# Optimization experiments

Measured on AMD Instinct MI355X. Metric: run time of the kernel, lower is better.

## Reference

```python
import jax, jax.numpy as jnp
import numpy as np

NUM_HEADS = 8
EPS = 1e-5


def setup_inputs() -> dict:
    key = jax.random.key(0)
    ks = jax.random.split(key, 7)
    B, C, H, W, D = 1, 256, 16, 16, 16
    return {
        "x": jax.random.normal(ks[0], (B, C, H, W, D), dtype=jnp.float32),
        "w_dw": jax.random.normal(ks[1], (C, 1, 3, 3, 3), dtype=jnp.float32) * 0.05,
        "b_dw": jax.random.normal(ks[2], (C,), dtype=jnp.float32) * 0.05,
        "w_qkv": jax.random.normal(ks[3], (3 * C, C), dtype=jnp.float32) * 0.05,
        "b_qkv": jax.random.normal(ks[4], (3 * C,), dtype=jnp.float32) * 0.05,
        "w_proj": jax.random.normal(ks[5], (C, C), dtype=jnp.float32) * 0.05,
        "b_proj": jax.random.normal(ks[6], (C,), dtype=jnp.float32) * 0.05,
    }


def reference(x, w_dw, b_dw, w_qkv, b_qkv, w_proj, b_proj):
    B, C, H, W, D = x.shape
    nh = NUM_HEADS
    hd = C // nh
    scale = hd ** (-0.5)
    N = H * W * D

    # depthwise 3x3x3 conv (groups=C), SAME padding
    y = jax.lax.conv_general_dilated(
        x, w_dw, window_strides=(1, 1, 1), padding="SAME",
        dimension_numbers=("NCHWD", "OIHWD", "NCHWD"),
        feature_group_count=C,
    ) + b_dw[None, :, None, None, None]

    # InstanceNorm3d (affine=False): normalize over spatial dims per (b, c)
    mu = y.mean(axis=(2, 3, 4), keepdims=True)
    var = y.var(axis=(2, 3, 4), keepdims=True)
    y = (y - mu) * jax.lax.rsqrt(var + EPS)

    # 1x1x1 conv -> 3*C channels
    qkv = jnp.einsum("bchwd,oc->bohwd", y, w_qkv) + b_qkv[None, :, None, None, None]

    # [B, 3, nh, hd, N] -> q, k, v each [B, nh, N, hd]
    qkv = qkv.reshape(B, 3, nh, hd, N)
    q, k, v = jnp.transpose(qkv, (1, 0, 2, 4, 3))

    attn = jax.nn.softmax(jnp.einsum("bhnd,bhmd->bhnm", q, k) * scale, axis=-1)
    out = jnp.einsum("bhnm,bhmd->bhnd", attn, v)  # [B, nh, N, hd]

    # transpose(-1, -2) then reshape to [B, C, H, W, D]
    out = jnp.transpose(out, (0, 1, 3, 2)).reshape(B, C, H, W, D)

    # output 1x1x1 projection
    out = jnp.einsum("bchwd,oc->bohwd", out, w_proj) + b_proj[None, :, None, None, None]
    return out
```

## Files before the change

kernel.cpp:

```cpp
#include <hip/hip_runtime.h>
#include <hip/hip_bf16.h>

#define NSP 4096
#define QSC2 0.25503486f

typedef __attribute__((ext_vector_type(8))) short bf16x8;
typedef __attribute__((ext_vector_type(4))) float f32x4;
typedef __attribute__((ext_vector_type(16))) float f32x16;

__device__ __forceinline__ unsigned short f2bf(float f){
  union{float f;unsigned int u;}c; c.f=f;
  unsigned int r = c.u + 0x7fffu + ((c.u>>16)&1u);
  return (unsigned short)(r>>16);
}
__device__ __forceinline__ unsigned int pk2(float a, float b){
  __hip_bfloat162 p = __float22bfloat162_rn(make_float2(a, b));
  unsigned int r; __builtin_memcpy(&r, &p, 4); return r;
}
__device__ __forceinline__ ushort4 pk4(float a, float b, float c, float d){
  union { ushort4 u4; uint2 u2; } u;
  u.u2.x = pk2(a, b); u.u2.y = pk2(c, d);
  return u.u4;
}
__device__ __forceinline__ float bfu2f(unsigned short u){
  union { unsigned int i; float f; } c; c.i = ((unsigned int)u) << 16; return c.f;
}

__global__ __launch_bounds__(1024) void k_dwconv(
    const float* __restrict__ x,
    const float* __restrict__ wdw,
    unsigned short* __restrict__ ybn)
{
  const int c = blockIdx.x;
  const int tid = threadIdx.x;
  __shared__ float xs[4096];
  __shared__ float wsh[27];
  __shared__ float rs[16], rq[16];

  const float* xc = x + (size_t)c * NSP;
  *(float4*)&xs[tid*4] = ((const float4*)xc)[tid];
  if (tid < 27) wsh[tid] = wdw[c*27 + tid];
  __syncthreads();

  const int h = tid >> 6, w = (tid >> 2) & 15, d0 = (tid & 3) * 4;
  float acc[4] = {};
  #pragma unroll
  for (int kh = 0; kh < 3; kh++){
    const int hh = h + kh - 1;
    if ((unsigned)hh >= 16u) continue;
    #pragma unroll
    for (int kw = 0; kw < 3; kw++){
      const int ww = w + kw - 1;
      if ((unsigned)ww >= 16u) continue;
      const float* rowp = &xs[((hh << 4) + ww) << 4];
      float win[6];
      const float4 c0 = *(const float4*)&rowp[d0];
      win[1] = c0.x; win[2] = c0.y; win[3] = c0.z; win[4] = c0.w;
      win[0] = d0        ? rowp[d0 - 1] : 0.f;
      win[5] = (d0 < 12) ? rowp[d0 + 4] : 0.f;
      #pragma unroll
      for (int kd = 0; kd < 3; kd++){
        const float wv = wsh[kh*9 + kw*3 + kd];
        #pragma unroll
        for (int j = 0; j < 4; j++) acc[j] += wv * win[j + kd];
      }
    }
  }

  float sum = 0.f, sumsq = 0.f;
  #pragma unroll
  for (int j = 0; j < 4; j++){ sum += acc[j]; sumsq += acc[j]*acc[j]; }
  #pragma unroll
  for (int off = 32; off > 0; off >>= 1){
    sum   += __shfl_down(sum, off, 64);
    sumsq += __shfl_down(sumsq, off, 64);
  }
  const int wid = tid >> 6, lane = tid & 63;
  if (lane == 0){ rs[wid] = sum; rq[wid] = sumsq; }
  __syncthreads();
  float ts = 0.f, tq = 0.f;
  #pragma unroll
  for (int i = 0; i < 16; i++){ ts += rs[i]; tq += rq[i]; }
  const float mean = ts * (1.f/4096.f);
  const float var  = tq * (1.f/4096.f) - mean*mean;
  const float rinv = rsqrtf(var + 1e-5f);

  *(ushort4*)(ybn + (size_t)c * NSP + tid*4) =
      pk4((acc[0]-mean)*rinv, (acc[1]-mean)*rinv, (acc[2]-mean)*rinv, (acc[3]-mean)*rinv);
}

__global__ __launch_bounds__(256) void k_qkv(
    const float* __restrict__ wqkv,
    const float* __restrict__ bqkv,
    const unsigned short* __restrict__ ybn,
    unsigned short* __restrict__ qb, unsigned short* __restrict__ kb,
    unsigned short* __restrict__ vbt)
{
  __shared__ unsigned short Wb[64][264];
  __shared__ unsigned short Ys[64][264];
  __shared__ float bsh[64];
  const int tid = threadIdx.x;
  const int o0 = blockIdx.y * 64;
  const int n0 = blockIdx.x * 64;
  {
    const int row = tid & 63, part = tid >> 6;
    const float* src = wqkv + (size_t)(o0 + row) * 256 + part * 64;
    unsigned short* dst = &Wb[row][part*64];
    #pragma unroll
    for (int j = 0; j < 8; j++){
      const float4 a = ((const float4*)src)[2*j];
      const float4 b = ((const float4*)src)[2*j+1];
      *(ushort4*)&dst[j*8]     = pk4(a.x, a.y, a.z, a.w);
      *(ushort4*)&dst[j*8 + 4] = pk4(b.x, b.y, b.z, b.w);
    }
    if (tid < 64) bsh[tid] = bqkv[o0 + tid];
  }
  {
    const int cl = tid >> 4, n4 = (tid & 15) * 4;
    #pragma unroll
    for (int i = 0; i < 16; i++){
      const int c = cl * 16 + i;
      const ushort4 v = *(const ushort4*)(ybn + (size_t)c * NSP + n0 + n4);
      Ys[n4+0][c] = v.x; Ys[n4+1][c] = v.y; Ys[n4+2][c] = v.z; Ys[n4+3][c] = v.w;
    }
  }
  __syncthreads();

  const int w = tid >> 6, lane = tid & 63, quad = lane >> 4, cc = lane & 15;
  const int nbase = n0 + w*16;
  const bool isv = (o0 >= 512);
  f32x4 acc[4] = {};

  #pragma unroll
  for (int k = 0; k < 8; k++){
    const bf16x8 y0 = *(const bf16x8*)&Ys[w*16 + cc][k*32 + quad*8];
    #pragma unroll
    for (int os = 0; os < 4; os++){
      const bf16x8 wf = *(const bf16x8*)&Wb[os*16 + cc][k*32 + quad*8];
      if (!isv) acc[os] = __builtin_amdgcn_mfma_f32_16x16x32_bf16(wf, y0, acc[os], 0, 0, 0);
      else      acc[os] = __builtin_amdgcn_mfma_f32_16x16x32_bf16(y0, wf, acc[os], 0, 0, 0);
    }
  }

  if (!isv){
    #pragma unroll
    for (int os = 0; os < 4; os++){
      const int obase = o0 + os*16 + quad*4;
      const int g = obase >> 8, hh = (obase >> 5) & 7, dd0 = obase & 31;
      const int n = nbase + cc;
      unsigned short* dst = (g == 0) ? qb : kb;
      const float sc = (g == 0) ? QSC2 : 1.f;
      const int bb = os*16 + quad*4;
      *(ushort4*)&dst[((size_t)hh * NSP + n) * 32 + dd0] =
          pk4((acc[os][0] + bsh[bb+0]) * sc, (acc[os][1] + bsh[bb+1]) * sc,
              (acc[os][2] + bsh[bb+2]) * sc, (acc[os][3] + bsh[bb+3]) * sc);
    }
  } else {
    #pragma unroll
    for (int os = 0; os < 4; os++){
      const int orow = o0 - 512 + os*16 + cc;
      const float bias = bsh[os*16 + cc];
      const int n4 = nbase + quad*4;
      *(ushort4*)&vbt[(size_t)orow * NSP + n4] =
          pk4(acc[os][0] + bias, acc[os][1] + bias, acc[os][2] + bias, acc[os][3] + bias);
    }
  }
}

__global__ __launch_bounds__(256) void k_attn(
    const unsigned short* __restrict__ qb,
    const unsigned short* __restrict__ kb,
    const unsigned short* __restrict__ vbt,
    unsigned short* __restrict__ opb, float* __restrict__ lp, int ktlen)
{
  const int h = blockIdx.y, q0 = blockIdx.x * 128, z = blockIdx.z;
  const int tid = threadIdx.x;
  const int w = tid >> 6, l = tid & 63;
  const int lq = l & 31, lb = l >> 5;

  __shared__ unsigned short ks [64][40];
  __shared__ unsigned short vsT[32][72];
  __shared__ unsigned short pst[128][72];

  const int qg = q0 + w*32 + lq;
  const bf16x8 qf0 = *(const bf16x8*)(qb + ((size_t)(h*NSP + qg))*32 + lb*8);
  const bf16x8 qf1 = *(const bf16x8*)(qb + ((size_t)(h*NSP + qg))*32 + 16 + lb*8);
  const unsigned short* kbase = kb  + (size_t)h * NSP * 32;
  const unsigned short* vbase = vbt + (size_t)h * 32 * NSP;

  f32x16 oacc = {};
  float lsum = 0.f;

  const int kt0 = z * ktlen;
  const int krow = tid >> 2, kseg = (tid & 3) * 8;
  const int vrow = tid >> 3, vseg = (tid & 7) * 8;
  const int iters = ktlen >> 6;

  for (int it = 0; it < iters; it++){
    const int kt = kt0 + it * 64;
    {
      *(uint4*)&ks[krow][kseg]  = *(const uint4*)(kbase + (size_t)(kt + krow) * 32 + kseg);
      *(uint4*)&vsT[vrow][vseg] = *(const uint4*)(vbase + (size_t)vrow * NSP + kt + vseg);
    }
    __syncthreads();

    #pragma unroll
    for (int t2 = 0; t2 < 2; t2++){
      const bf16x8 af0 = *(const bf16x8*)&ks[t2*32 + lq][lb*8];
      const bf16x8 af1 = *(const bf16x8*)&ks[t2*32 + lq][16 + lb*8];
      f32x16 sa = {};
      sa = __builtin_amdgcn_mfma_f32_32x32x16_bf16(af0, qf0, sa, 0, 0, 0);
      sa = __builtin_amdgcn_mfma_f32_32x32x16_bf16(af1, qf1, sa, 0, 0, 0);
      #pragma unroll
      for (int g = 0; g < 4; g++){
        const float p0 = __builtin_amdgcn_exp2f(sa[g*4+0]);
        const float p1 = __builtin_amdgcn_exp2f(sa[g*4+1]);
        const float p2 = __builtin_amdgcn_exp2f(sa[g*4+2]);
        const float p3 = __builtin_amdgcn_exp2f(sa[g*4+3]);
        lsum += (p0 + p1) + (p2 + p3);
        *(ushort4*)&pst[w*32 + lq][t2*32 + g*8 + lb*4] = pk4(p0, p1, p2, p3);
      }
    }
    #pragma unroll
    for (int ck = 0; ck < 4; ck++){
      const bf16x8 vf = *(const bf16x8*)&vsT[lq]       [ck*16 + lb*8];
      const bf16x8 pf = *(const bf16x8*)&pst[w*32 + lq][ck*16 + lb*8];
      oacc = __builtin_amdgcn_mfma_f32_32x32x16_bf16(vf, pf, oacc, 0, 0, 0);
    }
    __syncthreads();
  }

  lsum += __shfl_xor(lsum, 32, 64);

  unsigned short* dst = opb + ((size_t)z * NSP + qg) * 256 + h*32;
  #pragma unroll
  for (int g = 0; g < 4; g++){
    *(ushort4*)(dst + g*8 + lb*4) =
        pk4(oacc[g*4+0], oacc[g*4+1], oacc[g*4+2], oacc[g*4+3]);
  }
  if (lb == 0) lp[((size_t)z * 8 + h) * NSP + qg] = lsum;
}

__global__ __launch_bounds__(256) void k_proj(
    const float* __restrict__ wproj,
    const float* __restrict__ bproj,
    const unsigned short* __restrict__ opb,
    const float* __restrict__ lp,
    float* __restrict__ out, int nz)
{
  __shared__ unsigned short Wb[32][264];
  const int tid = threadIdx.x;
  const int o0 = blockIdx.y * 32;
  const int n0 = blockIdx.x * 64;
  {
    const int row = tid & 31, part = tid >> 5;
    const float* src = wproj + (size_t)(o0 + row) * 256 + part * 32;
    unsigned short* dst = &Wb[row][part*32];
    #pragma unroll
    for (int j = 0; j < 4; j++){
      const float4 a = ((const float4*)src)[2*j];
      const float4 b = ((const float4*)src)[2*j+1];
      *(ushort4*)&dst[j*8]     = pk4(a.x, a.y, a.z, a.w);
      *(ushort4*)&dst[j*8 + 4] = pk4(b.x, b.y, b.z, b.w);
    }
  }
  __syncthreads();

  const int w = tid >> 6, lane = tid & 63, quad = lane >> 4, cc = lane & 15;
  const int nbase = n0 + w*16;
  const int nr = nbase + cc;
  f32x4 acc[2] = {};

  #pragma unroll
  for (int k = 0; k < 8; k++){
    float lt = 0.f;
    float s[8] = {};
    for (int z = 0; z < nz; z++){
      lt += lp[((size_t)z*8 + k) * NSP + nr];
      union { uint4 q; unsigned short u[8]; } v;
      v.q = *(const uint4*)(opb + ((size_t)z * NSP + nr) * 256 + k*32 + quad*8);
      #pragma unroll
      for (int j = 0; j < 8; j++) s[j] += bfu2f(v.u[j]);
    }
    const float r = 1.f / lt;
    union { bf16x8 v; ushort4 u[2]; } yb;
    yb.u[0] = pk4(s[0]*r, s[1]*r, s[2]*r, s[3]*r);
    yb.u[1] = pk4(s[4]*r, s[5]*r, s[6]*r, s[7]*r);
    #pragma unroll
    for (int os = 0; os < 2; os++){
      const bf16x8 wf = *(const bf16x8*)&Wb[os*16 + cc][k*32 + quad*8];
      acc[os] = __builtin_amdgcn_mfma_f32_16x16x32_bf16(yb.v, wf, acc[os], 0, 0, 0);
    }
  }

  #pragma unroll
  for (int os = 0; os < 2; os++){
    const int o = o0 + os*16 + cc;
    const float bias = bproj[o];
    const int n4 = nbase + quad*4;
    *(float4*)&out[(size_t)o * NSP + n4] =
        make_float4(acc[os][0] + bias, acc[os][1] + bias,
                    acc[os][2] + bias, acc[os][3] + bias);
  }
}

extern "C" void kernel_launch(void* const* d_in, const int* in_sizes, int n_in,
                              void* d_out, int out_size, void* d_ws, size_t ws_size,
                              hipStream_t stream) {
  (void)in_sizes; (void)n_in; (void)out_size;
  const float* x     = (const float*)d_in[0];
  const float* wdw   = (const float*)d_in[1];
  const float* bdw   = (const float*)d_in[2];  (void)bdw;
  const float* wqkv  = (const float*)d_in[3];
  const float* bqkv  = (const float*)d_in[4];
  const float* wproj = (const float*)d_in[5];
  const float* bproj = (const float*)d_in[6];
  float* out = (float*)d_out;

  const int nz = (ws_size >= ((size_t)16 << 20)) ? 4 : 2;
  const int ktlen = NSP / nz;

  char* ws = (char*)d_ws;
  const size_t opB = (size_t)nz << 21;
  unsigned short* opb = (unsigned short*)ws;
  unsigned short* ybn = (unsigned short*)ws;
  unsigned short* qb  = (unsigned short*)(ws + opB);
  unsigned short* kb  = (unsigned short*)(ws + opB + (2<<20));
  unsigned short* vbt = (unsigned short*)(ws + opB + (4<<20));
  float*          lp  = (float*)(ws + opB + (6<<20));

  k_dwconv <<<dim3(256),        dim3(1024), 0, stream>>>(x, wdw, ybn);
  k_qkv    <<<dim3(64, 12),     dim3(256),  0, stream>>>(wqkv, bqkv, ybn, qb, kb, vbt);
  k_attn   <<<dim3(32, 8, nz),  dim3(256),  0, stream>>>(qb, kb, vbt, opb, lp, ktlen);
  k_proj   <<<dim3(64, 8),      dim3(256),  0, stream>>>(wproj, bproj, opb, lp, out, nz);
}
```

Before: 140.5 us.

## Fuse all stages into one cooperative persistent kernel with grid syncs

Replaces the four separate launches with a single cooperative kernel of 512 blocks that runs depthwise conv, instance-norm stats, QKV GEMM, attention and projection as phases separated by grid-wide syncs. The conv is split across two blocks per channel, with partial stats exchanged through global memory. The aim is to remove per-launch overhead and inter-kernel gaps. In exchange it adds grid barrier costs and caps parallelism at 512 resident blocks, so attention tasks are looped per block. It falls back to the old four launches if the cooperative launch fails.

```diff
diff --git a/kernel.cpp b/kernel.cpp
--- a/kernel.cpp
+++ b/kernel.cpp
@@ -1,5 +1,8 @@
 #include <hip/hip_runtime.h>
 #include <hip/hip_bf16.h>
+#include <hip/hip_cooperative_groups.h>
+
+namespace cg = cooperative_groups;
 
 #define NSP 4096
 #define QSC2 0.25503486f
@@ -26,9 +29,291 @@
   union { unsigned int i; float f; } c; c.i = ((unsigned int)u) << 16; return c.f;
 }
 
+struct FParams {
+  const float* x; const float* wdw;
+  const float* wqkv; const float* bqkv;
+  const float* wproj; const float* bproj;
+  unsigned short* ybn; unsigned short* qb; unsigned short* kb; unsigned short* vbt;
+  unsigned short* opb; float* lp; float2* stats;
+  float* out; int nz; int ktlen;
+};
+
+__global__ __launch_bounds__(256) void k_fused(FParams p)
+{
+  __shared__ __align__(16) char smem[67840];
+  cg::grid_group gg = cg::this_grid();
+  const int tid = threadIdx.x;
+  const int bid = blockIdx.x;
+  const int w = tid >> 6, lane = tid & 63, quad = lane >> 4, cc = lane & 15;
+
+  float a8[8];
+  {
+    float* xs  = (float*)smem;
+    float* wsh = (float*)(smem + 16384);
+    float* rs  = (float*)(smem + 16512);
+    float* rq  = (float*)(smem + 16544);
+    const int c = bid >> 1, half = bid & 1;
+    const float* xc = p.x + (size_t)c * NSP;
+    #pragma unroll
+    for (int i = 0; i < 4; i++)
+      *(float4*)&xs[(i*256 + tid)*4] = ((const float4*)xc)[i*256 + tid];
+    if (tid < 27) wsh[tid] = p.wdw[c*27 + tid];
+    __syncthreads();
+
+    const int h = half*8 + (tid >> 5), ww0 = (tid >> 1) & 15, d0 = (tid & 1) * 8;
+    #pragma unroll
+    for (int j = 0; j < 8; j++) a8[j] = 0.f;
+    #pragma unroll
+    for (int kh = 0; kh < 3; kh++){
+      const int hh = h + kh - 1;
+      if ((unsigned)hh >= 16u) continue;
+      #pragma unroll
+      for (int kw = 0; kw < 3; kw++){
+        const int ww = ww0 + kw - 1;
+        if ((unsigned)ww >= 16u) continue;
+        const float* rowp = &xs[((hh << 4) + ww) << 4];
+        float win[10];
+        const float4 c0 = *(const float4*)&rowp[d0];
+        const float4 c1 = *(const float4*)&rowp[d0 + 4];
+        win[1] = c0.x; win[2] = c0.y; win[3] = c0.z; win[4] = c0.w;
+        win[5] = c1.x; win[6] = c1.y; win[7] = c1.z; win[8] = c1.w;
+        win[0] = d0 ? rowp[7] : 0.f;
+        win[9] = d0 ? 0.f : rowp[8];
+        #pragma unroll
+        for (int kd = 0; kd < 3; kd++){
+          const float wv = wsh[kh*9 + kw*3 + kd];
+          #pragma unroll
+          for (int j = 0; j < 8; j++) a8[j] += wv * win[j + kd];
+        }
+      }
+    }
+    float sum = 0.f, sumsq = 0.f;
+    #pragma unroll
+    for (int j = 0; j < 8; j++){ sum += a8[j]; sumsq += a8[j]*a8[j]; }
+    #pragma unroll
+    for (int off = 32; off > 0; off >>= 1){
+      sum   += __shfl_down(sum, off, 64);
+      sumsq += __shfl_down(sumsq, off, 64);
+    }
+    if (lane == 0){ rs[w] = sum; rq[w] = sumsq; }
+    __syncthreads();
+    if (tid == 0)
+      p.stats[bid] = make_float2(rs[0]+rs[1]+rs[2]+rs[3], rq[0]+rq[1]+rq[2]+rq[3]);
+  }
+  gg.sync();
+
+  {
+    const int c = bid >> 1, half = bid & 1;
+    const float2 s0 = p.stats[bid & ~1], s1 = p.stats[bid | 1];
+    const float mean = (s0.x + s1.x) * (1.f/4096.f);
+    const float var  = (s0.y + s1.y) * (1.f/4096.f) - mean*mean;
+    const float rinv = rsqrtf(var + 1e-5f);
+    const int h = half*8 + (tid >> 5), ww0 = (tid >> 1) & 15, d0 = (tid & 1) * 8;
+    unsigned short* yo = p.ybn + (size_t)c * NSP + (h << 8) + (ww0 << 4) + d0;
+    *(ushort4*)yo =
+        pk4((a8[0]-mean)*rinv, (a8[1]-mean)*rinv, (a8[2]-mean)*rinv, (a8[3]-mean)*rinv);
+    *(ushort4*)(yo + 4) =
+        pk4((a8[4]-mean)*rinv, (a8[5]-mean)*rinv, (a8[6]-mean)*rinv, (a8[7]-mean)*rinv);
+  }
+  gg.sync();
+
+  {
+    unsigned short (*Ys)[264] = (unsigned short (*)[264])smem;
+    unsigned short (*Wb)[264] = (unsigned short (*)[264])(smem + 33792);
+    float* bsh = (float*)(smem + 67584);
+    const int nt = bid >> 3, oslot = bid & 7;
+    const int n0 = nt * 64;
+    {
+      const int cl = tid >> 4, n4 = (tid & 15) * 4;
+      #pragma unroll
+      for (int i = 0; i < 16; i++){
+        const int c = cl*16 + i;
+        const ushort4 v = *(const ushort4*)(p.ybn + (size_t)c * NSP + n0 + n4);
+        Ys[n4+0][c] = v.x; Ys[n4+1][c] = v.y; Ys[n4+2][c] = v.z; Ys[n4+3][c] = v.w;
+      }
+    }
+    const int numo = (oslot < 4) ? 2 : 1;
+    for (int oi = 0; oi < numo; oi++){
+      const int o0 = (oslot + oi*8) * 64;
+      __syncthreads();
+      {
+        const int row = tid & 63, part = tid >> 6;
+        const float* src = p.wqkv + (size_t)(o0 + row) * 256 + part * 64;
+        unsigned short* dst = &Wb[row][part*64];
+        #pragma unroll
+        for (int j = 0; j < 8; j++){
+          const float4 a = ((const float4*)src)[2*j];
+          const float4 b = ((const float4*)src)[2*j+1];
+          *(ushort4*)&dst[j*8]     = pk4(a.x, a.y, a.z, a.w);
+          *(ushort4*)&dst[j*8 + 4] = pk4(b.x, b.y, b.z, b.w);
+        }
+        if (tid < 64) bsh[tid] = p.bqkv[o0 + tid];
+      }
+      __syncthreads();
+
+      const int nbase = n0 + w*16;
+      const bool isv = (o0 >= 512);
+      f32x4 acc[4] = {};
+      #pragma unroll
+      for (int k = 0; k < 8; k++){
+        const bf16x8 y0 = *(const bf16x8*)&Ys[w*16 + cc][k*32 + quad*8];
+        #pragma unroll
+        for (int os = 0; os < 4; os++){
+          const bf16x8 wf = *(const bf16x8*)&Wb[os*16 + cc][k*32 + quad*8];
+          if (!isv) acc[os] = __builtin_amdgcn_mfma_f32_16x16x32_bf16(wf, y0, acc[os], 0, 0, 0);
+          else      acc[os] = __builtin_amdgcn_mfma_f32_16x16x32_bf16(y0, wf, acc[os], 0, 0, 0);
+        }
+      }
+      if (!isv){
+        #pragma unroll
+        for (int os = 0; os < 4; os++){
+          const int obase = o0 + os*16 + quad*4;
+          const int g = obase >> 8, hh = (obase >> 5) & 7, dd0 = obase & 31;
+          const int n = nbase + cc;
+          unsigned short* dst = (g == 0) ? p.qb : p.kb;
+          const float sc = (g == 0) ? QSC2 : 1.f;
+          const int bb = os*16 + quad*4;
+          *(ushort4*)&dst[((size_t)hh * NSP + n) * 32 + dd0] =
+              pk4((acc[os][0] + bsh[bb+0]) * sc, (acc[os][1] + bsh[bb+1]) * sc,
+                  (acc[os][2] + bsh[bb+2]) * sc, (acc[os][3] + bsh[bb+3]) * sc);
+        }
+      } else {
+        #pragma unroll
+        for (int os = 0; os < 4; os++){
+          const int orow = o0 - 512 + os*16 + cc;
+          const float bias = bsh[os*16 + cc];
+          const int n4 = nbase + quad*4;
+          *(ushort4*)&p.vbt[(size_t)orow * NSP + n4] =
+              pk4(acc[os][0] + bias, acc[os][1] + bias, acc[os][2] + bias, acc[os][3] + bias);
+        }
+      }
+    }
+  }
+  gg.sync();
+
+  {
+    unsigned short (*ks)[40]  = (unsigned short (*)[40])smem;
+    unsigned short (*vsT)[72] = (unsigned short (*)[72])(smem + 5120);
+    unsigned short (*pst)[72] = (unsigned short (*)[72])(smem + 9728);
+    const int lq = lane & 31, lb = lane >> 5;
+    const int krow = tid >> 2, kseg = (tid & 3) * 8;
+    const int vrow = tid >> 3, vseg = (tid & 7) * 8;
+    const int ntask = p.nz << 8;
+
+    for (int t = bid; t < ntask; t += 512){
+      const int qx = t & 31, h = (t >> 5) & 7, z = t >> 8;
+      const int q0 = qx * 128;
+      const int qg = q0 + w*32 + lq;
+      const bf16x8 qf0 = *(const bf16x8*)(p.qb + ((size_t)(h*NSP + qg))*32 + lb*8);
+      const bf16x8 qf1 = *(const bf16x8*)(p.qb + ((size_t)(h*NSP + qg))*32 + 16 + lb*8);
+      const unsigned short* kbase = p.kb  + (size_t)h * NSP * 32;
+      const unsigned short* vbase = p.vbt + (size_t)h * 32 * NSP;
+
+      f32x16 oacc = {};
+      float lsum = 0.f;
+      const int kt0 = z * p.ktlen;
+      const int iters = p.ktlen >> 6;
+      __syncthreads();
+
+      for (int it = 0; it < iters; it++){
+        const int kt = kt0 + it * 64;
+        *(uint4*)&ks[krow][kseg]  = *(const uint4*)(kbase + (size_t)(kt + krow) * 32 + kseg);
+        *(uint4*)&vsT[vrow][vseg] = *(const uint4*)(vbase + (size_t)vrow * NSP + kt + vseg);
+        __syncthreads();
+
+        #pragma unroll
+        for (int t2 = 0; t2 < 2; t2++){
+          const bf16x8 af0 = *(const bf16x8*)&ks[t2*32 + lq][lb*8];
+          const bf16x8 af1 = *(const bf16x8*)&ks[t2*32 + lq][16 + lb*8];
+          f32x16 sa = {};
+          sa = __builtin_amdgcn_mfma_f32_32x32x16_bf16(af0, qf0, sa, 0, 0, 0);
+          sa = __builtin_amdgcn_mfma_f32_32x32x16_bf16(af1, qf1, sa, 0, 0, 0);
+          #pragma unroll
+          for (int g = 0; g < 4; g++){
+            const float p0 = __builtin_amdgcn_exp2f(sa[g*4+0]);
+            const float p1 = __builtin_amdgcn_exp2f(sa[g*4+1]);
+            const float p2 = __builtin_amdgcn_exp2f(sa[g*4+2]);
+            const float p3 = __builtin_amdgcn_exp2f(sa[g*4+3]);
+            lsum += (p0 + p1) + (p2 + p3);
+            *(ushort4*)&pst[w*32 + lq][t2*32 + g*8 + lb*4] = pk4(p0, p1, p2, p3);
+          }
+        }
+        #pragma unroll
+        for (int ck = 0; ck < 4; ck++){
+          const bf16x8 vf = *(const bf16x8*)&vsT[lq]       [ck*16 + lb*8];
+          const bf16x8 pf = *(const bf16x8*)&pst[w*32 + lq][ck*16 + lb*8];
+          oacc = __builtin_amdgcn_mfma_f32_32x32x16_bf16(vf, pf, oacc, 0, 0, 0);
+        }
+        __syncthreads();
+      }
+
+      lsum += __shfl_xor(lsum, 32, 64);
+      unsigned short* dst = p.opb + ((size_t)z * NSP + qg) * 256 + h*32;
+      #pragma unroll
+      for (int g = 0; g < 4; g++){
+        *(ushort4*)(dst + g*8 + lb*4) =
+            pk4(oacc[g*4+0], oacc[g*4+1], oacc[g*4+2], oacc[g*4+3]);
+      }
+      if (lb == 0) p.lp[((size_t)z * 8 + h) * NSP + qg] = lsum;
+    }
+  }
+  gg.sync();
+
+  {
+    unsigned short (*Wb)[264] = (unsigned short (*)[264])smem;
+    const int n0 = (bid & 63) * 64, o0 = (bid >> 6) * 32;
+    {
+      const int row = tid & 31, part = tid >> 5;
+      const float* src = p.wproj + (size_t)(o0 + row) * 256 + part * 32;
+      unsigned short* dst = &Wb[row][part*32];
+      #pragma unroll
+      for (int j = 0; j < 4; j++){
+        const float4 a = ((const float4*)src)[2*j];
+        const float4 b = ((const float4*)src)[2*j+1];
+        *(ushort4*)&dst[j*8]     = pk4(a.x, a.y, a.z, a.w);
+        *(ushort4*)&dst[j*8 + 4] = pk4(b.x, b.y, b.z, b.w);
+      }
+    }
+    __syncthreads();
+
+    const int nbase = n0 + w*16;
+    const int nr = nbase + cc;
+    f32x4 acc[2] = {};
+    #pragma unroll
+    for (int k = 0; k < 8; k++){
+      float lt = 0.f;
+      float s[8] = {};
+      for (int z = 0; z < p.nz; z++){
+        lt += p.lp[((size_t)z*8 + k) * NSP + nr];
+        union { uint4 q; unsigned short u[8]; } v;
+        v.q = *(const uint4*)(p.opb + ((size_t)z * NSP + nr) * 256 + k*32 + quad*8);
+        #pragma unroll
+        for (int j = 0; j < 8; j++) s[j] += bfu2f(v.u[j]);
+      }
+      const float r = 1.f / lt;
+      union { bf16x8 v; ushort4 u[2]; } yb;
+      yb.u[0] = pk4(s[0]*r, s[1]*r, s[2]*r, s[3]*r);
+      yb.u[1] = pk4(s[4]*r, s[5]*r, s[6]*r, s[7]*r);
+      #pragma unroll
+      for (int os = 0; os < 2; os++){
+        const bf16x8 wf = *(const bf16x8*)&Wb[os*16 + cc][k*32 + quad*8];
+        acc[os] = __builtin_amdgcn_mfma_f32_16x16x32_bf16(yb.v, wf, acc[os], 0, 0, 0);
+      }
+    }
+    #pragma unroll
+    for (int os = 0; os < 2; os++){
+      const int o = o0 + os*16 + cc;
+      const float bias = p.bproj[o];
+      const int n4 = nbase + quad*4;
+      *(float4*)&p.out[(size_t)o * NSP + n4] =
+          make_float4(acc[os][0] + bias, acc[os][1] + bias,
+                      acc[os][2] + bias, acc[os][3] + bias);
+    }
+  }
+}
+
 __global__ __launch_bounds__(1024) void k_dwconv(
-    const float* __restrict__ x,
-    const float* __restrict__ wdw,
+    const float* __restrict__ x, const float* __restrict__ wdw,
     unsigned short* __restrict__ ybn)
 {
   const int c = blockIdx.x;
@@ -36,12 +321,10 @@
   __shared__ float xs[4096];
   __shared__ float wsh[27];
   __shared__ float rs[16], rq[16];
-
   const float* xc = x + (size_t)c * NSP;
   *(float4*)&xs[tid*4] = ((const float4*)xc)[tid];
   if (tid < 27) wsh[tid] = wdw[c*27 + tid];
   __syncthreads();
-
   const int h = tid >> 6, w = (tid >> 2) & 15, d0 = (tid & 3) * 4;
   float acc[4] = {};
   #pragma unroll
@@ -66,7 +349,6 @@
       }
     }
   }
-
   float sum = 0.f, sumsq = 0.f;
   #pragma unroll
   for (int j = 0; j < 4; j++){ sum += acc[j]; sumsq += acc[j]*acc[j]; }
@@ -84,14 +366,12 @@
   const float mean = ts * (1.f/4096.f);
   const float var  = tq * (1.f/4096.f) - mean*mean;
   const float rinv = rsqrtf(var + 1e-5f);
-
   *(ushort4*)(ybn + (size_t)c * NSP + tid*4) =
       pk4((acc[0]-mean)*rinv, (acc[1]-mean)*rinv, (acc[2]-mean)*rinv, (acc[3]-mean)*rinv);
 }
 
 __global__ __launch_bounds__(256) void k_qkv(
-    const float* __restrict__ wqkv,
-    const float* __restrict__ bqkv,
+    const float* __restrict__ wqkv, const float* __restrict__ bqkv,
     const unsigned short* __restrict__ ybn,
     unsigned short* __restrict__ qb, unsigned short* __restrict__ kb,
     unsigned short* __restrict__ vbt)
@@ -125,12 +405,10 @@
     }
   }
   __syncthreads();
-
   const int w = tid >> 6, lane = tid & 63, quad = lane >> 4, cc = lane & 15;
   const int nbase = n0 + w*16;
   const bool isv = (o0 >= 512);
   f32x4 acc[4] = {};
-
   #pragma unroll
   for (int k = 0; k < 8; k++){
     const bf16x8 y0 = *(const bf16x8*)&Ys[w*16 + cc][k*32 + quad*8];
@@ -141,7 +419,6 @@
       else      acc[os] = __builtin_amdgcn_mfma_f32_16x16x32_bf16(y0, wf, acc[os], 0, 0, 0);
     }
   }
-
   if (!isv){
     #pragma unroll
     for (int os = 0; os < 4; os++){
@@ -177,33 +454,25 @@
   const int tid = threadIdx.x;
   const int w = tid >> 6, l = tid & 63;
   const int lq = l & 31, lb = l >> 5;
-
   __shared__ unsigned short ks [64][40];
   __shared__ unsigned short vsT[32][72];
   __shared__ unsigned short pst[128][72];
-
   const int qg = q0 + w*32 + lq;
   const bf16x8 qf0 = *(const bf16x8*)(qb + ((size_t)(h*NSP + qg))*32 + lb*8);
   const bf16x8 qf1 = *(const bf16x8*)(qb + ((size_t)(h*NSP + qg))*32 + 16 + lb*8);
   const unsigned short* kbase = kb  + (size_t)h * NSP * 32;
   const unsigned short* vbase = vbt + (size_t)h * 32 * NSP;
-
   f32x16 oacc = {};
   float lsum = 0.f;
-
   const int kt0 = z * ktlen;
   const int krow = tid >> 2, kseg = (tid & 3) * 8;
   const int vrow = tid >> 3, vseg = (tid & 7) * 8;
   const int iters = ktlen >> 6;
-
   for (int it = 0; it < iters; it++){
     const int kt = kt0 + it * 64;
-    {
-      *(uint4*)&ks[krow][kseg]  = *(const uint4*)(kbase + (size_t)(kt + krow) * 32 + kseg);
-      *(uint4*)&vsT[vrow][vseg] = *(const uint4*)(vbase + (size_t)vrow * NSP + kt + vseg);
-    }
+    *(uint4*)&ks[krow][kseg]  = *(const uint4*)(kbase + (size_t)(kt + krow) * 32 + kseg);
+    *(uint4*)&vsT[vrow][vseg] = *(const uint4*)(vbase + (size_t)vrow * NSP + kt + vseg);
     __syncthreads();
-
     #pragma unroll
     for (int t2 = 0; t2 < 2; t2++){
       const bf16x8 af0 = *(const bf16x8*)&ks[t2*32 + lq][lb*8];
@@ -229,9 +498,7 @@
     }
     __syncthreads();
   }
-
   lsum += __shfl_xor(lsum, 32, 64);
-
   unsigned short* dst = opb + ((size_t)z * NSP + qg) * 256 + h*32;
   #pragma unroll
   for (int g = 0; g < 4; g++){
@@ -242,10 +509,8 @@
 }
 
 __global__ __launch_bounds__(256) void k_proj(
-    const float* __restrict__ wproj,
-    const float* __restrict__ bproj,
-    const unsigned short* __restrict__ opb,
-    const float* __restrict__ lp,
+    const float* __restrict__ wproj, const float* __restrict__ bproj,
+    const unsigned short* __restrict__ opb, const float* __restrict__ lp,
     float* __restrict__ out, int nz)
 {
   __shared__ unsigned short Wb[32][264];
@@ -265,12 +530,10 @@
     }
   }
   __syncthreads();
-
   const int w = tid >> 6, lane = tid & 63, quad = lane >> 4, cc = lane & 15;
   const int nbase = n0 + w*16;
   const int nr = nbase + cc;
   f32x4 acc[2] = {};
-
   #pragma unroll
   for (int k = 0; k < 8; k++){
     float lt = 0.f;
@@ -292,7 +555,6 @@
       acc[os] = __builtin_amdgcn_mfma_f32_16x16x32_bf16(yb.v, wf, acc[os], 0, 0, 0);
     }
   }
-
   #pragma unroll
   for (int os = 0; os < 2; os++){
     const int o = o0 + os*16 + cc;
@@ -328,9 +590,23 @@
   unsigned short* kb  = (unsigned short*)(ws + opB + (2<<20));
   unsigned short* vbt = (unsigned short*)(ws + opB + (4<<20));
   float*          lp  = (float*)(ws + opB + (6<<20));
-
-  k_dwconv <<<dim3(256),        dim3(1024), 0, stream>>>(x, wdw, ybn);
-  k_qkv    <<<dim3(64, 12),     dim3(256),  0, stream>>>(wqkv, bqkv, ybn, qb, kb, vbt);
-  k_attn   <<<dim3(32, 8, nz),  dim3(256),  0, stream>>>(qb, kb, vbt, opb, lp, ktlen);
-  k_proj   <<<dim3(64, 8),      dim3(256),  0, stream>>>(wproj, bproj, opb, lp, out, nz);
-}
+  float2*         stats = (float2*)(ws + opB + (6<<20) + ((size_t)nz << 17));
+
+  FParams hp;
+  hp.x = x; hp.wdw = wdw; hp.wqkv = wqkv; hp.bqkv = bqkv;
+  hp.wproj = wproj; hp.bproj = bproj;
+  hp.ybn = ybn; hp.qb = qb; hp.kb = kb; hp.vbt = vbt;
+  hp.opb = opb; hp.lp = lp; hp.stats = stats; hp.out = out;
+  hp.nz = nz; hp.ktlen = ktlen;
+  void* kargs[] = { (void*)&hp };
+
+  hipError_t err = hipLaunchCooperativeKernel(
+      (const void*)k_fused, dim3(512), dim3(256), kargs, 0, stream);
+  if (err != hipSuccess){
+    (void)hipGetLastError();
+    k_dwconv <<<dim3(256),       dim3(1024), 0, stream>>>(x, wdw, ybn);
+    k_qkv    <<<dim3(64, 12),    dim3(256),  0, stream>>>(wqkv, bqkv, ybn, qb, kb, vbt);
+    k_attn   <<<dim3(32, 8, nz), dim3(256),  0, stream>>>(qb, kb, vbt, opb, lp, ktlen);
+    k_proj   <<<dim3(64, 8),     dim3(256),  0, stream>>>(wproj, bproj, opb, lp, out, nz);
+  }
+}
```

New measurement: 395.7 us. 2.82x slower.
